# Kernel optimization log

Hardware: AMD Instinct MI355X
Metric: run time of the kernel (lower is better)

## Reference

```python
import jax, jax.numpy as jnp
import numpy as np

B, S, D, H, HD, NU, T = 64, 512, 256, 4, 64, 100000, 24


def setup_inputs() -> dict:
    key = jax.random.key(0)
    ks = jax.random.split(key, 13)
    return {
        "timeslot_embedded": jax.random.normal(ks[0], (T, D), jnp.float32),
        "user": jax.random.randint(ks[1], (B,), 0, NU, dtype=jnp.int64) if jax.config.jax_enable_x64 else jax.random.randint(ks[1], (B,), 0, NU, dtype=jnp.int32),
        "hour": jax.random.randint(ks[2], (B, S), 0, T, dtype=jnp.int32),
        "hour_mask": jax.random.randint(ks[3], (B, S, T), 0, 2, dtype=jnp.int32),
        "user_pref": jax.random.normal(ks[4], (NU, D), jnp.float32) * 0.02,
        "Wq": jax.random.normal(ks[5], (H, HD, 2 * D), jnp.float32) * 0.02,
        "bq": jnp.zeros((H, HD), jnp.float32),
        "Wk": jax.random.normal(ks[6], (H, HD, D), jnp.float32) * 0.02,
        "bk": jnp.zeros((H, HD), jnp.float32),
        "Wv": jax.random.normal(ks[7], (H, HD, D), jnp.float32) * 0.02,
        "bv": jnp.zeros((H, HD), jnp.float32),
        "Wu": jax.random.normal(ks[8], (D, D), jnp.float32) * 0.02,
        "bu": jnp.zeros((D,), jnp.float32),
    }


def reference(timeslot_embedded, user, hour, hour_mask, user_pref,
              Wq, bq, Wk, bk, Wv, bv, Wu, bu):
    b, s = hour.shape
    n = b * s
    # per-token features
    user_feat = jnp.broadcast_to(user_pref[user][:, None, :], (b, s, D)).reshape(n, D)
    time_feat = timeslot_embedded[hour.reshape(n)]          # [N, D]
    query = jnp.concatenate([user_feat, time_feat], axis=-1)  # [N, 2D]
    # all heads at once (equivalent to the per-head Linear loop)
    q = jnp.einsum('nd,hkd->nhk', query, Wq) + bq[None]               # [N, H, HD]
    k = jnp.einsum('td,hkd->htk', timeslot_embedded, Wk) + bk[:, None, :]  # [H, T, HD]
    v = jnp.einsum('td,hkd->htk', timeslot_embedded, Wv) + bv[:, None, :]  # [H, T, HD]
    scale = 1.0 / np.sqrt(HD).astype(np.float32)
    scores = jnp.einsum('nhk,htk->nht', q, k) * scale                 # [N, H, T]
    mask = hour_mask.reshape(n, T)[:, None, :]                        # [N, 1, T]
    scores = jnp.where(mask == 1, -jnp.inf, scores)
    attn = jax.nn.softmax(scores, axis=-1)
    out = jnp.einsum('nht,htk->nhk', attn, v).reshape(n, H * HD)      # concat heads
    out = out @ Wu.T + bu
    return out.reshape(b, s, D)
```

## Files before the change

### kernel.cpp

```cpp
#include <hip/hip_runtime.h>
#include <hip/hip_bf16.h>

#define QU_OFF   0
#define KK_OFF   16384
#define ET_OFF   22528
#define VWB_OFF  24832

typedef __attribute__((ext_vector_type(8))) short bf16x8;
typedef __attribute__((ext_vector_type(4))) float f32x4;

__device__ __forceinline__ unsigned short f2bf(float f) {
    unsigned u = __builtin_bit_cast(unsigned, f);
    return (unsigned short)((u + 0x7FFFu + ((u >> 16) & 1u)) >> 16);
}
__device__ __forceinline__ unsigned packbf(float a, float b) {
    return (unsigned)f2bf(a) | ((unsigned)f2bf(b) << 16);
}
__device__ __forceinline__ bf16x8 cvt8(float4 f0, float4 f1) {
    int4 v = make_int4(packbf(f0.x, f0.y), packbf(f0.z, f0.w),
                       packbf(f1.x, f1.y), packbf(f1.z, f1.w));
    return __builtin_bit_cast(bf16x8, v);
}
__device__ __forceinline__ float dot4(float4 a, float4 b, float s) {
    return fmaf(a.x, b.x, fmaf(a.y, b.y, fmaf(a.z, b.z, fmaf(a.w, b.w, s))));
}


__global__ __launch_bounds__(256) void precomp(
    const float* __restrict__ ts, const int* __restrict__ user,
    const float* __restrict__ user_pref,
    const float* __restrict__ Wq, const float* __restrict__ bq,
    const float* __restrict__ Wk, const float* __restrict__ bk,
    const float* __restrict__ Wv, const float* __restrict__ bv,
    const float* __restrict__ Wu, float* __restrict__ ws)
{
    __shared__ unsigned sA[4096];
    __shared__ float sM1[32 * 68];
    __shared__ float sM2[32 * 68];
    int tid = threadIdx.x, blk = blockIdx.x;
    int w = tid >> 6, l = tid & 63;
    int eo = (l >> 4) * 8;

    if (blk < 8) {
        int q = blk >> 1, nh = blk & 1, b0 = q * 16;
        for (int u = tid; u < 512; u += 256) {
            int r = u >> 5, e0 = (u & 31) * 8;
            const float* src = user_pref + (size_t)user[b0 + r] * 256 + e0;
            float4 f0 = *(const float4*)src, f1 = *(const float4*)(src + 4);
            unsigned* dst = &sA[(((e0 >> 5) * 2) * 64 + (r & 15) + 16 * ((e0 >> 3) & 3)) * 4];
            dst[0] = packbf(f0.x, f0.y); dst[1] = packbf(f0.z, f0.w);
            dst[2] = packbf(f1.x, f1.y); dst[3] = packbf(f1.z, f1.w);
        }
        __syncthreads();
        #pragma unroll
        for (int ntq = 0; ntq < 2; ++ntq) {
            int col = nh * 128 + (w * 2 + ntq) * 16 + (l & 15);
            float4 fb[8][2];
            #pragma unroll
            for (int kt = 0; kt < 8; ++kt) {
                const float* Bp = Wq + (size_t)col * 512 + kt * 32 + eo;
                fb[kt][0] = *(const float4*)Bp; fb[kt][1] = *(const float4*)(Bp + 4);
            }
            f32x4 acc = (f32x4)0.f;
            #pragma unroll
            for (int kt = 0; kt < 8; ++kt) {
                bf16x8 afr = __builtin_bit_cast(bf16x8, *(const int4*)&sA[((kt * 2) * 64 + l) * 4]);
                acc = __builtin_amdgcn_mfma_f32_16x16x32_bf16(afr, cvt8(fb[kt][0], fb[kt][1]), acc, 0, 0, 0);
            }
            int row = (l >> 4) * 4;
            #pragma unroll
            for (int r = 0; r < 4; ++r)
                ws[QU_OFF + (size_t)(b0 + row + r) * 256 + col] = acc[r];
        }
        return;
    }

    for (int u = tid; u < 768; u += 256) {
        int r = u >> 5, e0 = (u & 31) * 8;
        const float* src = ts + r * 256 + e0;
        float4 f0 = *(const float4*)src, f1 = *(const float4*)(src + 4);
        unsigned* dst = &sA[(((e0 >> 5) * 2 + (r >> 4)) * 64 + (r & 15) + 16 * ((e0 >> 3) & 3)) * 4];
        dst[0] = packbf(f0.x, f0.y); dst[1] = packbf(f0.z, f0.w);
        dst[2] = packbf(f1.x, f1.y); dst[3] = packbf(f1.z, f1.w);
    }
    __syncthreads();

    if (blk < 12) {
        int h = blk - 8;
        int j = h * 64 + w * 16 + (l & 15);
        float4 fa[8][2], fc[8][2];
        #pragma unroll
        for (int kt = 0; kt < 8; ++kt) {
            const float* Bq = Wq + (size_t)j * 512 + 256 + kt * 32 + eo;
            const float* Bk = Wk + (size_t)j * 256 + kt * 32 + eo;
            fa[kt][0] = *(const float4*)Bq; fa[kt][1] = *(const float4*)(Bq + 4);
            fc[kt][0] = *(const float4*)Bk; fc[kt][1] = *(const float4*)(Bk + 4);
        }
        f32x4 aca[2] = {(f32x4)0.f, (f32x4)0.f};
        f32x4 acb[2] = {(f32x4)0.f, (f32x4)0.f};
        #pragma unroll
        for (int kt = 0; kt < 8; ++kt) {
            bf16x8 bq8 = cvt8(fa[kt][0], fa[kt][1]);
            bf16x8 bk8 = cvt8(fc[kt][0], fc[kt][1]);
            #pragma unroll
            for (int mt = 0; mt < 2; ++mt) {
                bf16x8 afr = __builtin_bit_cast(bf16x8, *(const int4*)&sA[((kt * 2 + mt) * 64 + l) * 4]);
                aca[mt] = __builtin_amdgcn_mfma_f32_16x16x32_bf16(afr, bq8, aca[mt], 0, 0, 0);
                acb[mt] = __builtin_amdgcn_mfma_f32_16x16x32_bf16(afr, bk8, acb[mt], 0, 0, 0);
            }
        }
        float bqv = bq[j], bkv = bk[j];
        int hd = w * 16 + (l & 15);
        #pragma unroll
        for (int mt = 0; mt < 2; ++mt) {
            int t0 = mt * 16 + (l >> 4) * 4;
            #pragma unroll
            for (int r = 0; r < 4; ++r) {
                int t = t0 + r;
                if (t < 24) {
                    sM1[t * 68 + hd] = aca[mt][r] + bqv;
                    float kv = acb[mt][r] + bkv;
                    sM2[t * 68 + hd] = kv;
                    ws[KK_OFF + (h * 24 + t) * 64 + hd] = kv;
                }
            }
        }
        __syncthreads();
        for (int u = tid; u < 576; u += 256) {
            int tp = u / 24, t = u - tp * 24;
            const float4* qp4 = (const float4*)&sM1[tp * 68];
            const float4* kp4 = (const float4*)&sM2[t * 68];
            float s = 0.f;
            #pragma unroll
            for (int i = 0; i < 16; ++i) s = dot4(qp4[i], kp4[i], s);
            ws[ET_OFF + tp * 96 + h * 24 + t] = expf(s * 0.125f);
        }
        return;
    }

    {
        int h = blk - 12;
        int jv = h * 64 + w * 16 + (l & 15);
        float4 fv[8][2];
        #pragma unroll
        for (int kt = 0; kt < 8; ++kt) {
            const float* Bv = Wv + (size_t)jv * 256 + kt * 32 + eo;
            fv[kt][0] = *(const float4*)Bv; fv[kt][1] = *(const float4*)(Bv + 4);
        }
        f32x4 acv[2] = {(f32x4)0.f, (f32x4)0.f};
        #pragma unroll
        for (int kt = 0; kt < 8; ++kt) {
            bf16x8 bv8 = cvt8(fv[kt][0], fv[kt][1]);
            #pragma unroll
            for (int mt = 0; mt < 2; ++mt) {
                bf16x8 afr = __builtin_bit_cast(bf16x8, *(const int4*)&sA[((kt * 2 + mt) * 64 + l) * 4]);
                acv[mt] = __builtin_amdgcn_mfma_f32_16x16x32_bf16(afr, bv8, acv[mt], 0, 0, 0);
            }
        }
        float bvv = bv[jv];
        int hd = w * 16 + (l & 15);
        #pragma unroll
        for (int mt = 0; mt < 2; ++mt) {
            int t0 = mt * 16 + (l >> 4) * 4;
            #pragma unroll
            for (int r = 0; r < 4; ++r)
                if (t0 + r < 24) sM1[(t0 + r) * 68 + hd] = acv[mt][r] + bvv;
        }
        __syncthreads();
        f32x4 ac2[2][4];
        #pragma unroll
        for (int mt = 0; mt < 2; ++mt)
            #pragma unroll
            for (int q = 0; q < 4; ++q) ac2[mt][q] = (f32x4)0.f;
        #pragma unroll
        for (int kt2 = 0; kt2 < 2; ++kt2) {
            int k0 = kt2 * 32 + eo;
            bf16x8 a2[2];
            #pragma unroll
            for (int mt = 0; mt < 2; ++mt) {
                int m = mt * 16 + (l & 15);
                float4 g0 = *(const float4*)&sM1[m * 68 + k0];
                float4 g1 = *(const float4*)&sM1[m * 68 + k0 + 4];
                a2[mt] = cvt8(g0, g1);
            }
            float4 fu[4][2];
            #pragma unroll
            for (int q = 0; q < 4; ++q) {
                int d = (w * 4 + q) * 16 + (l & 15);
                const float* Bu = Wu + (size_t)d * 256 + h * 64 + k0;
                fu[q][0] = *(const float4*)Bu; fu[q][1] = *(const float4*)(Bu + 4);
            }
            #pragma unroll
            for (int q = 0; q < 4; ++q) {
                bf16x8 bu8 = cvt8(fu[q][0], fu[q][1]);
                #pragma unroll
                for (int mt = 0; mt < 2; ++mt)
                    ac2[mt][q] = __builtin_amdgcn_mfma_f32_16x16x32_bf16(a2[mt], bu8, ac2[mt][q], 0, 0, 0);
            }
        }
        unsigned* vwb = (unsigned*)(ws + VWB_OFF);
        #pragma unroll
        for (int mt = 0; mt < 2; ++mt) {
            int t0 = mt * 16 + (l >> 4) * 4;
            if (t0 < 24) {
                #pragma unroll
                for (int q = 0; q < 4; ++q) {
                    int d = (w * 4 + q) * 16 + (l & 15);
                    #pragma unroll
                    for (int pp = 0; pp < 2; ++pp) {
                        int ht = h * 24 + t0 + pp * 2;
                        unsigned pk = packbf(ac2[mt][q][pp * 2], ac2[mt][q][pp * 2 + 1]);
                        int ktC = ht >> 5, ntC = d >> 4;
                        int lgC = (ht >> 3) & 3, jhC = (ht & 7) >> 1;
                        vwb[(ktC * 16 + ntC) * 256 + ((d & 15) + 16 * lgC) * 4 + jhC] = pk;
                    }
                }
            }
        }
    }
}

__global__ __launch_bounds__(256) void attn_mfma(
    const int* __restrict__ hour, const int* __restrict__ hour_mask,
    const float* __restrict__ ws, const float* __restrict__ bu,
    float* __restrict__ out)
{
    const float* ET = ws + ET_OFF;
    __shared__ int4 A_lds[12 * 64];
    __shared__ float EU_s[96];
    int tid = threadIdx.x;
    int nb = blockIdx.x * 64;
    int b = nb >> 9;
    if (tid < 96) {
        const float4* qp = (const float4*)(ws + QU_OFF + b * 256 + (tid / 24) * 64);
        const float4* kp = (const float4*)(ws + KK_OFF + tid * 64);
        float s = 0.f;
        #pragma unroll
        for (int i = 0; i < 16; ++i) s = dot4(qp[i], kp[i], s);
        EU_s[tid] = expf(s * 0.125f);
    }
    __syncthreads();
    {
        int tok = tid >> 2, h = tid & 3;
        int n = nb + tok;
        int th = hour[n];
        const float4* EUp = (const float4*)(EU_s + h * 24);
        const float4* ETp = (const float4*)(ET + th * 96 + h * 24);
        const int4*   mp  = (const int4*)(hour_mask + (long long)n * 24);
        float p[24]; float ssum = 0.f;
        #pragma unroll
        for (int q = 0; q < 6; ++q) {
            float4 e = EUp[q]; float4 f = ETp[q]; int4 m = mp[q];
            float v0 = (m.x != 0) ? 0.f : e.x * f.x;
            float v1 = (m.y != 0) ? 0.f : e.y * f.y;
            float v2 = (m.z != 0) ? 0.f : e.z * f.z;
            float v3 = (m.w != 0) ? 0.f : e.w * f.w;
            p[q*4+0] = v0; p[q*4+1] = v1; p[q*4+2] = v2; p[q*4+3] = v3;
            ssum += (v0 + v1) + (v2 + v3);
        }
        float r = 1.0f / ssum;
        int mt = tok >> 4, tl = tok & 15;
        #pragma unroll
        for (int tp = 0; tp < 12; ++tp) {
            int ht = h * 24 + tp * 2;
            unsigned pack = packbf(p[tp*2] * r, p[tp*2+1] * r);
            int kt = ht >> 5, lg = (ht >> 3) & 3, jh = (ht & 7) >> 1;
            ((unsigned*)A_lds)[((kt * 4 + mt) * 64 + tl + 16 * lg) * 4 + jh] = pack;
        }
    }
    __syncthreads();
    int w = tid >> 6, l = tid & 63;
    const int4* Bg = (const int4*)(ws + VWB_OFF);
    bf16x8 afr[3][4], bfr[3][4];
    #pragma unroll
    for (int kt = 0; kt < 3; ++kt)
        #pragma unroll
        for (int q = 0; q < 4; ++q) {
            afr[kt][q] = __builtin_bit_cast(bf16x8, A_lds[(kt * 4 + q) * 64 + l]);
            bfr[kt][q] = __builtin_bit_cast(bf16x8, Bg[(kt * 16 + w * 4 + q) * 64 + l]);
        }
    f32x4 acc[4][4];
    #pragma unroll
    for (int mt = 0; mt < 4; ++mt)
        #pragma unroll
        for (int q = 0; q < 4; ++q) acc[mt][q] = (f32x4)0.f;
    #pragma unroll
    for (int kt = 0; kt < 3; ++kt)
        #pragma unroll
        for (int mt = 0; mt < 4; ++mt)
            #pragma unroll
            for (int q = 0; q < 4; ++q)
                acc[mt][q] = __builtin_amdgcn_mfma_f32_16x16x32_bf16(
                    afr[kt][mt], bfr[kt][q], acc[mt][q], 0, 0, 0);
    int colb = w * 64 + (l & 15);
    float buv[4];
    #pragma unroll
    for (int q = 0; q < 4; ++q) buv[q] = bu[colb + q * 16];
    int row0 = nb + (l >> 4) * 4;
    #pragma unroll
    for (int mt = 0; mt < 4; ++mt)
        #pragma unroll
        for (int q = 0; q < 4; ++q) {
            float* op = out + (size_t)(row0 + mt * 16) * 256 + colb + q * 16;
            #pragma unroll
            for (int r = 0; r < 4; ++r)
                op[(size_t)r * 256] = acc[mt][q][r] + buv[q];
        }
}

extern "C" void kernel_launch(void* const* d_in, const int* in_sizes, int n_in,
                              void* d_out, int out_size, void* d_ws, size_t ws_size,
                              hipStream_t stream)
{
    const float* ts        = (const float*)d_in[0];
    const int*   user      = (const int*)  d_in[1];
    const int*   hour      = (const int*)  d_in[2];
    const int*   hour_mask = (const int*)  d_in[3];
    const float* user_pref = (const float*)d_in[4];
    const float* Wq        = (const float*)d_in[5];
    const float* bq        = (const float*)d_in[6];
    const float* Wk        = (const float*)d_in[7];
    const float* bk        = (const float*)d_in[8];
    const float* Wv        = (const float*)d_in[9];
    const float* bv        = (const float*)d_in[10];
    const float* Wu        = (const float*)d_in[11];
    const float* bu        = (const float*)d_in[12];
    float* ws  = (float*)d_ws;
    float* out = (float*)d_out;

    hipLaunchKernelGGL(precomp, dim3(16), dim3(256), 0, stream,
                       ts, user, user_pref, Wq, bq, Wk, bk, Wv, bv, Wu, ws);
    hipLaunchKernelGGL(attn_mfma, dim3(512), dim3(256), 0, stream,
                       hour, hour_mask, ws, bu, out);
}
```

Before: 24.65 us.

## Widen attention blocks, stage output through LDS for coalesced stores, split precomp

The attention kernel now runs 512-thread blocks covering 128 tokens, with two M-halves sharing the B fragments. Mask, hour, ET and V*Wu fragments are loaded before the first barrier so their latency overlaps the EU computation. Outputs are staged through a per-wave LDS tile and written as row-contiguous float4 nontemporal stores instead of strided scalar stores. The precomp kernel spreads the user-query projection over 16 blocks instead of 8 to shorten its critical path. The cost is more LDS and register pressure, and fewer blocks in the attention grid.

```diff
diff --git a/kernel.cpp b/kernel.cpp
--- a/kernel.cpp
+++ b/kernel.cpp
@@ -8,6 +8,7 @@
 
 typedef __attribute__((ext_vector_type(8))) short bf16x8;
 typedef __attribute__((ext_vector_type(4))) float f32x4;
+typedef __attribute__((ext_vector_type(4))) int   i32x4;
 
 __device__ __forceinline__ unsigned short f2bf(float f) {
     unsigned u = __builtin_bit_cast(unsigned, f);
@@ -23,6 +24,9 @@
 }
 __device__ __forceinline__ float dot4(float4 a, float4 b, float s) {
     return fmaf(a.x, b.x, fmaf(a.y, b.y, fmaf(a.z, b.z, fmaf(a.w, b.w, s))));
+}
+__device__ __forceinline__ float dot4v(f32x4 a, f32x4 b, float s) {
+    return fmaf(a[0], b[0], fmaf(a[1], b[1], fmaf(a[2], b[2], fmaf(a[3], b[3], s))));
 }
 
 
@@ -41,8 +45,8 @@
     int w = tid >> 6, l = tid & 63;
     int eo = (l >> 4) * 8;
 
-    if (blk < 8) {
-        int q = blk >> 1, nh = blk & 1, b0 = q * 16;
+    if (blk < 16) {
+        int q = blk >> 2, co = (blk & 3) * 64, b0 = q * 16;
         for (int u = tid; u < 512; u += 256) {
             int r = u >> 5, e0 = (u & 31) * 8;
             const float* src = user_pref + (size_t)user[b0 + r] * 256 + e0;
@@ -52,26 +56,23 @@
             dst[2] = packbf(f1.x, f1.y); dst[3] = packbf(f1.z, f1.w);
         }
         __syncthreads();
-        #pragma unroll
-        for (int ntq = 0; ntq < 2; ++ntq) {
-            int col = nh * 128 + (w * 2 + ntq) * 16 + (l & 15);
-            float4 fb[8][2];
-            #pragma unroll
-            for (int kt = 0; kt < 8; ++kt) {
-                const float* Bp = Wq + (size_t)col * 512 + kt * 32 + eo;
-                fb[kt][0] = *(const float4*)Bp; fb[kt][1] = *(const float4*)(Bp + 4);
-            }
-            f32x4 acc = (f32x4)0.f;
-            #pragma unroll
-            for (int kt = 0; kt < 8; ++kt) {
-                bf16x8 afr = __builtin_bit_cast(bf16x8, *(const int4*)&sA[((kt * 2) * 64 + l) * 4]);
-                acc = __builtin_amdgcn_mfma_f32_16x16x32_bf16(afr, cvt8(fb[kt][0], fb[kt][1]), acc, 0, 0, 0);
-            }
-            int row = (l >> 4) * 4;
-            #pragma unroll
-            for (int r = 0; r < 4; ++r)
-                ws[QU_OFF + (size_t)(b0 + row + r) * 256 + col] = acc[r];
-        }
+        int col = co + w * 16 + (l & 15);
+        float4 fb[8][2];
+        #pragma unroll
+        for (int kt = 0; kt < 8; ++kt) {
+            const float* Bp = Wq + (size_t)col * 512 + kt * 32 + eo;
+            fb[kt][0] = *(const float4*)Bp; fb[kt][1] = *(const float4*)(Bp + 4);
+        }
+        f32x4 acc = (f32x4)0.f;
+        #pragma unroll
+        for (int kt = 0; kt < 8; ++kt) {
+            bf16x8 afr = __builtin_bit_cast(bf16x8, *(const int4*)&sA[((kt * 2) * 64 + l) * 4]);
+            acc = __builtin_amdgcn_mfma_f32_16x16x32_bf16(afr, cvt8(fb[kt][0], fb[kt][1]), acc, 0, 0, 0);
+        }
+        int row = (l >> 4) * 4;
+        #pragma unroll
+        for (int r = 0; r < 4; ++r)
+            ws[QU_OFF + (size_t)(b0 + row + r) * 256 + col] = acc[r];
         return;
     }
 
@@ -85,8 +86,8 @@
     }
     __syncthreads();
 
-    if (blk < 12) {
-        int h = blk - 8;
+    if (blk < 20) {
+        int h = blk - 16;
         int j = h * 64 + w * 16 + (l & 15);
         float4 fa[8][2], fc[8][2];
         #pragma unroll
@@ -139,7 +140,7 @@
     }
 
     {
-        int h = blk - 12;
+        int h = blk - 20;
         int jv = h * 64 + w * 16 + (l & 15);
         float4 fv[8][2];
         #pragma unroll
@@ -220,65 +221,76 @@
     }
 }
 
-__global__ __launch_bounds__(256) void attn_mfma(
+__global__ __launch_bounds__(512) void attn_mfma(
     const int* __restrict__ hour, const int* __restrict__ hour_mask,
     const float* __restrict__ ws, const float* __restrict__ bu,
     float* __restrict__ out)
 {
     const float* ET = ws + ET_OFF;
-    __shared__ int4 A_lds[12 * 64];
+    __shared__ int4 A_lds[24 * 64];
     __shared__ float EU_s[96];
-    int tid = threadIdx.x;
-    int nb = blockIdx.x * 64;
+    __shared__ __align__(16) float stg[8 * 1088];
+    int tid = threadIdx.x, w = tid >> 6, l = tid & 63;
+    int mh = w >> 2, ns = w & 3;
+    int nb = blockIdx.x * 128;
     int b = nb >> 9;
+
+    int tok = tid >> 2, h = tid & 3, n = nb + tok;
+    int th = hour[n];
+    const i32x4* mp = (const i32x4*)(hour_mask + (long long)n * 24);
+    i32x4 msk[6];
+    #pragma unroll
+    for (int q = 0; q < 6; ++q) msk[q] = __builtin_nontemporal_load(mp + q);
+    const int4* Bg = (const int4*)(ws + VWB_OFF);
+    int4 breg[12];
+    #pragma unroll
+    for (int kt = 0; kt < 3; ++kt)
+        #pragma unroll
+        for (int q = 0; q < 4; ++q)
+            breg[kt * 4 + q] = Bg[(kt * 16 + ns * 4 + q) * 64 + l];
     if (tid < 96) {
-        const float4* qp = (const float4*)(ws + QU_OFF + b * 256 + (tid / 24) * 64);
-        const float4* kp = (const float4*)(ws + KK_OFF + tid * 64);
+        const f32x4* qp = (const f32x4*)(ws + QU_OFF + b * 256 + (tid / 24) * 64);
+        const f32x4* kp = (const f32x4*)(ws + KK_OFF + tid * 64);
         float s = 0.f;
         #pragma unroll
-        for (int i = 0; i < 16; ++i) s = dot4(qp[i], kp[i], s);
+        for (int i = 0; i < 16; ++i) s = dot4v(qp[i], kp[i], s);
         EU_s[tid] = expf(s * 0.125f);
     }
+    const f32x4* ETp = (const f32x4*)(ET + th * 96 + h * 24);
+    f32x4 fET[6];
+    #pragma unroll
+    for (int q = 0; q < 6; ++q) fET[q] = ETp[q];
     __syncthreads();
     {
-        int tok = tid >> 2, h = tid & 3;
-        int n = nb + tok;
-        int th = hour[n];
-        const float4* EUp = (const float4*)(EU_s + h * 24);
-        const float4* ETp = (const float4*)(ET + th * 96 + h * 24);
-        const int4*   mp  = (const int4*)(hour_mask + (long long)n * 24);
+        const f32x4* EUp = (const f32x4*)(EU_s + h * 24);
         float p[24]; float ssum = 0.f;
         #pragma unroll
         for (int q = 0; q < 6; ++q) {
-            float4 e = EUp[q]; float4 f = ETp[q]; int4 m = mp[q];
-            float v0 = (m.x != 0) ? 0.f : e.x * f.x;
-            float v1 = (m.y != 0) ? 0.f : e.y * f.y;
-            float v2 = (m.z != 0) ? 0.f : e.z * f.z;
-            float v3 = (m.w != 0) ? 0.f : e.w * f.w;
+            f32x4 e = EUp[q]; f32x4 f = fET[q]; i32x4 mm = msk[q];
+            float v0 = (mm[0] != 0) ? 0.f : e[0] * f[0];
+            float v1 = (mm[1] != 0) ? 0.f : e[1] * f[1];
+            float v2 = (mm[2] != 0) ? 0.f : e[2] * f[2];
+            float v3 = (mm[3] != 0) ? 0.f : e[3] * f[3];
             p[q*4+0] = v0; p[q*4+1] = v1; p[q*4+2] = v2; p[q*4+3] = v3;
             ssum += (v0 + v1) + (v2 + v3);
         }
         float r = 1.0f / ssum;
-        int mt = tok >> 4, tl = tok & 15;
+        int mt8 = tok >> 4, tl = tok & 15;
         #pragma unroll
         for (int tp = 0; tp < 12; ++tp) {
             int ht = h * 24 + tp * 2;
             unsigned pack = packbf(p[tp*2] * r, p[tp*2+1] * r);
             int kt = ht >> 5, lg = (ht >> 3) & 3, jh = (ht & 7) >> 1;
-            ((unsigned*)A_lds)[((kt * 4 + mt) * 64 + tl + 16 * lg) * 4 + jh] = pack;
+            ((unsigned*)A_lds)[((kt * 8 + mt8) * 64 + tl + 16 * lg) * 4 + jh] = pack;
         }
     }
     __syncthreads();
-    int w = tid >> 6, l = tid & 63;
-    const int4* Bg = (const int4*)(ws + VWB_OFF);
-    bf16x8 afr[3][4], bfr[3][4];
+    bf16x8 afr[3][4];
     #pragma unroll
     for (int kt = 0; kt < 3; ++kt)
         #pragma unroll
-        for (int q = 0; q < 4; ++q) {
-            afr[kt][q] = __builtin_bit_cast(bf16x8, A_lds[(kt * 4 + q) * 64 + l]);
-            bfr[kt][q] = __builtin_bit_cast(bf16x8, Bg[(kt * 16 + w * 4 + q) * 64 + l]);
-        }
+        for (int q = 0; q < 4; ++q)
+            afr[kt][q] = __builtin_bit_cast(bf16x8, A_lds[(kt * 8 + mh * 4 + q) * 64 + l]);
     f32x4 acc[4][4];
     #pragma unroll
     for (int mt = 0; mt < 4; ++mt)
@@ -291,21 +303,30 @@
             #pragma unroll
             for (int q = 0; q < 4; ++q)
                 acc[mt][q] = __builtin_amdgcn_mfma_f32_16x16x32_bf16(
-                    afr[kt][mt], bfr[kt][q], acc[mt][q], 0, 0, 0);
-    int colb = w * 64 + (l & 15);
-    float buv[4];
-    #pragma unroll
-    for (int q = 0; q < 4; ++q) buv[q] = bu[colb + q * 16];
-    int row0 = nb + (l >> 4) * 4;
-    #pragma unroll
-    for (int mt = 0; mt < 4; ++mt)
-        #pragma unroll
-        for (int q = 0; q < 4; ++q) {
-            float* op = out + (size_t)(row0 + mt * 16) * 256 + colb + q * 16;
+                    afr[kt][mt], __builtin_bit_cast(bf16x8, breg[kt * 4 + q]),
+                    acc[mt][q], 0, 0, 0);
+    float* sp = stg + w * 1088;
+    int rr = l >> 2, cg = l & 3;
+    f32x4 bu4[4];
+    #pragma unroll
+    for (int i = 0; i < 4; ++i)
+        bu4[i] = *(const f32x4*)(bu + ns * 64 + i * 16 + cg * 4);
+    int rbase = nb + mh * 64;
+    #pragma unroll
+    for (int mt = 0; mt < 4; ++mt) {
+        #pragma unroll
+        for (int q = 0; q < 4; ++q)
             #pragma unroll
             for (int r = 0; r < 4; ++r)
-                op[(size_t)r * 256] = acc[mt][q][r] + buv[q];
-        }
+                sp[((l >> 4) * 4 + r) * 68 + q * 16 + (l & 15)] = acc[mt][q][r];
+        float* orow = out + (size_t)(rbase + mt * 16 + rr) * 256 + ns * 64;
+        #pragma unroll
+        for (int i = 0; i < 4; ++i) {
+            f32x4 v = *(const f32x4*)(sp + rr * 68 + i * 16 + cg * 4);
+            v = v + bu4[i];
+            __builtin_nontemporal_store(v, (f32x4*)(orow + i * 16 + cg * 4));
+        }
+    }
 }
 
 extern "C" void kernel_launch(void* const* d_in, const int* in_sizes, int n_in,
@@ -328,8 +349,8 @@
     float* ws  = (float*)d_ws;
     float* out = (float*)d_out;
 
-    hipLaunchKernelGGL(precomp, dim3(16), dim3(256), 0, stream,
+    hipLaunchKernelGGL(precomp, dim3(24), dim3(256), 0, stream,
                        ts, user, user_pref, Wq, bq, Wk, bk, Wv, bv, Wu, ws);
-    hipLaunchKernelGGL(attn_mfma, dim3(512), dim3(256), 0, stream,
+    hipLaunchKernelGGL(attn_mfma, dim3(256), dim3(512), 0, stream,
                        hour, hour_mask, ws, bu, out);
 }
```

After: 24.70 us. No clear change (+0.2%).
